# Kernel tuning notes

Measured on AMD Instinct MI355X. Metric: run time of the kernel, lower is better.

## Reference

```python
import jax, jax.numpy as jnp
import numpy as np

NUM_WINDOWS = 162   # icosphere order-2 windows
NUM_HEADS = 8

def layernorm(x, g, b, eps=1e-5):
    m = jnp.mean(x, axis=-1, keepdims=True)
    v = jnp.var(x, axis=-1, keepdims=True)
    return (x - m) * jax.lax.rsqrt(v + eps) * g + b

def setup_inputs() -> dict:
    key = jax.random.key(0)
    ks = jax.random.split(key, 16)
    B, N, C = 1, 41472, 512
    H, hid = NUM_HEADS, 4 * 512
    s = 0.02
    # window assignment: 162 windows x 256 vertices, shuffled (gather-based partition)
    rng = np.random.default_rng(0)
    wid = np.repeat(np.arange(NUM_WINDOWS), N // NUM_WINDOWS)
    rng.shuffle(wid)
    return {
        "x": jax.random.normal(ks[0], (B, N, C), jnp.float32),
        "mesh": jax.random.normal(ks[1], (N, 3), jnp.float32),
        "ln1_g": jnp.ones((C,), jnp.float32),
        "ln1_b": jnp.zeros((C,), jnp.float32),
        "qkv_w": jax.random.normal(ks[2], (C, 3 * C), jnp.float32) * s,
        "qkv_b": jnp.zeros((3 * C,), jnp.float32),
        "rel_bias": jax.random.normal(ks[3], (H, 1, 1), jnp.float32) * s,
        "proj_w": jax.random.normal(ks[4], (C, C), jnp.float32) * s,
        "proj_b": jnp.zeros((C,), jnp.float32),
        "ln2_g": jnp.ones((C,), jnp.float32),
        "ln2_b": jnp.zeros((C,), jnp.float32),
        "ffn_w1": jax.random.normal(ks[5], (C, hid), jnp.float32) * s,
        "ffn_b1": jnp.zeros((hid,), jnp.float32),
        "ffn_w2": jax.random.normal(ks[6], (hid, C), jnp.float32) * s,
        "ffn_b2": jnp.zeros((C,), jnp.float32),
        "window_ids": jnp.asarray(wid, dtype=jnp.int32),
    }

def reference(x, mesh, ln1_g, ln1_b, qkv_w, qkv_b, rel_bias, proj_w, proj_b,
              ln2_g, ln2_b, ffn_w1, ffn_b1, ffn_w2, ffn_b2, window_ids):
    B, N, C = x.shape
    H = NUM_HEADS
    hd = C // H
    ws = N // NUM_WINDOWS
    # --- gather-based window partition ---
    idx = jnp.argsort(window_ids)                      # [N]
    w = x[:, idx, :].reshape(B * NUM_WINDOWS, ws, C)   # [BW, ws, C]
    # --- window attention on norm1(windows) ---
    h = layernorm(w, ln1_g, ln1_b)
    qkv = (h @ qkv_w + qkv_b).reshape(B * NUM_WINDOWS, ws, 3, H, hd)
    q, k, v = qkv[:, :, 0], qkv[:, :, 1], qkv[:, :, 2]  # [BW, ws, H, hd]
    scale = hd ** -0.5
    attn = jnp.einsum('wqhd,wkhd->whqk', q, k) * scale + rel_bias
    attn = jax.nn.softmax(attn, axis=-1)
    out = jnp.einsum('whqk,wkhd->wqhd', attn, v).reshape(B * NUM_WINDOWS, ws, C)
    out = out @ proj_w + proj_b
    # --- reverse partition + residual ---
    inv = jnp.argsort(idx)
    x = x + out.reshape(B, N, C)[:, inv, :]
    # --- FFN block ---
    h2 = layernorm(x, ln2_g, ln2_b)
    f = jax.nn.gelu(h2 @ ffn_w1 + ffn_b1, approximate=False) @ ffn_w2 + ffn_b2
    x = x + f
    return (x, mesh)
```

## Files before the change

kernel.cpp:

```cpp
#include <hip/hip_runtime.h>
#include <hip/hip_bf16.h>
#include <math.h>

#define NW   162
#define WS   256
#define NH   8
#define HD   64
#define CC   512
#define NTOK 41472
#define HID  2048

typedef __bf16 bf16x8 __attribute__((ext_vector_type(8)));
typedef float  floatx4 __attribute__((ext_vector_type(4)));

__device__ __forceinline__ void gload_lds16(const __bf16* g, __bf16* l) {
    __builtin_amdgcn_global_load_lds((const __attribute__((address_space(1))) void*)g,
                                     (__attribute__((address_space(3))) void*)l,
                                     16, 0, 0);
}
__device__ __forceinline__ float fast_rcp(float x) { return __builtin_amdgcn_rcpf(x); }

__global__ __launch_bounds__(256)
void build_perm_atomic(const int* __restrict__ wid, int* __restrict__ perm,
                       int* __restrict__ pos, int* __restrict__ counters) {
    const int i = blockIdx.x * 256 + threadIdx.x;
    const int w = wid[i];
    const int r = atomicAdd(&counters[w], 1);
    perm[w * WS + r] = i;
    pos[i] = w * WS + r;
}

__global__ void transpose_bf16(const float* __restrict__ in,
                               __bf16* __restrict__ out, int K, int N) {
    int idx = blockIdx.x * 256 + threadIdx.x;
    if (idx >= K * N) return;
    int n = idx / K, k = idx - n * K;
    out[idx] = (__bf16)in[(size_t)k * N + n];
}

__global__ __launch_bounds__(64)
void ln1_gather(const float* __restrict__ x, const int* __restrict__ perm,
                const float* __restrict__ g, const float* __restrict__ b,
                __bf16* __restrict__ h) {
    const int j = blockIdx.x, lane = threadIdx.x;
    const int orig = perm[j];
    const float4* xp = (const float4*)(x + (size_t)orig * CC);
    float4 a0 = xp[lane * 2 + 0], a1 = xp[lane * 2 + 1];
    float s  = a0.x + a0.y + a0.z + a0.w + a1.x + a1.y + a1.z + a1.w;
    float sq = a0.x*a0.x + a0.y*a0.y + a0.z*a0.z + a0.w*a0.w
             + a1.x*a1.x + a1.y*a1.y + a1.z*a1.z + a1.w*a1.w;
#pragma unroll
    for (int o = 32; o; o >>= 1) { s += __shfl_xor(s, o); sq += __shfl_xor(sq, o); }
    const float m  = s * (1.f / CC);
    const float rs = rsqrtf(sq * (1.f / CC) - m * m + 1e-5f);
    const float4* g4 = (const float4*)g;  const float4* b4 = (const float4*)b;
    float4 g0 = g4[lane*2+0], g1 = g4[lane*2+1], bb0 = b4[lane*2+0], bb1 = b4[lane*2+1];
    bf16x8 o8;
    o8[0] = (__bf16)((a0.x - m) * rs * g0.x + bb0.x);
    o8[1] = (__bf16)((a0.y - m) * rs * g0.y + bb0.y);
    o8[2] = (__bf16)((a0.z - m) * rs * g0.z + bb0.z);
    o8[3] = (__bf16)((a0.w - m) * rs * g0.w + bb0.w);
    o8[4] = (__bf16)((a1.x - m) * rs * g1.x + bb1.x);
    o8[5] = (__bf16)((a1.y - m) * rs * g1.y + bb1.y);
    o8[6] = (__bf16)((a1.z - m) * rs * g1.z + bb1.z);
    o8[7] = (__bf16)((a1.w - m) * rs * g1.w + bb1.w);
    *(bf16x8*)(h + (size_t)j * CC + lane * 8) = o8;
}

__global__ __launch_bounds__(64)
void resid_ln2(const float* __restrict__ x, const float* __restrict__ ptmp,
               const int* __restrict__ pos, const float* __restrict__ g,
               const float* __restrict__ b, float* __restrict__ xout,
               __bf16* __restrict__ h2) {
    const int i = blockIdx.x, lane = threadIdx.x;
    const int p = pos[i];
    const float4* xp = (const float4*)(x + (size_t)i * CC);
    const float4* pp = (const float4*)(ptmp + (size_t)p * CC);
    float4 a0 = xp[lane*2+0], a1 = xp[lane*2+1];
    float4 t0 = pp[lane*2+0], t1 = pp[lane*2+1];
    a0.x += t0.x; a0.y += t0.y; a0.z += t0.z; a0.w += t0.w;
    a1.x += t1.x; a1.y += t1.y; a1.z += t1.z; a1.w += t1.w;
    float4* op = (float4*)(xout + (size_t)i * CC);
    op[lane*2+0] = a0; op[lane*2+1] = a1;
    float s  = a0.x + a0.y + a0.z + a0.w + a1.x + a1.y + a1.z + a1.w;
    float sq = a0.x*a0.x + a0.y*a0.y + a0.z*a0.z + a0.w*a0.w
             + a1.x*a1.x + a1.y*a1.y + a1.z*a1.z + a1.w*a1.w;
#pragma unroll
    for (int o = 32; o; o >>= 1) { s += __shfl_xor(s, o); sq += __shfl_xor(sq, o); }
    const float m  = s * (1.f / CC);
    const float rs = rsqrtf(sq * (1.f / CC) - m * m + 1e-5f);
    const float4* g4 = (const float4*)g;  const float4* b4 = (const float4*)b;
    float4 g0 = g4[lane*2+0], g1 = g4[lane*2+1], bb0 = b4[lane*2+0], bb1 = b4[lane*2+1];
    bf16x8 o8;
    o8[0] = (__bf16)((a0.x - m) * rs * g0.x + bb0.x);
    o8[1] = (__bf16)((a0.y - m) * rs * g0.y + bb0.y);
    o8[2] = (__bf16)((a0.z - m) * rs * g0.z + bb0.z);
    o8[3] = (__bf16)((a0.w - m) * rs * g0.w + bb0.w);
    o8[4] = (__bf16)((a1.x - m) * rs * g1.x + bb1.x);
    o8[5] = (__bf16)((a1.y - m) * rs * g1.y + bb1.y);
    o8[6] = (__bf16)((a1.z - m) * rs * g1.z + bb1.z);
    o8[7] = (__bf16)((a1.w - m) * rs * g1.w + bb1.w);
    *(bf16x8*)(h2 + (size_t)i * CC + lane * 8) = o8;
}

template <int EPI>
__global__ __launch_bounds__(256)
void gemm_bt(const __bf16* __restrict__ A, const __bf16* __restrict__ Bt,
             const float* __restrict__ bias, const float* __restrict__ res,
             float* __restrict__ Cf, __bf16* __restrict__ Cb,
             int M, int N, int K) {
    __shared__ __bf16 As[128 * 64];
    __shared__ __bf16 Bs[128 * 64];
    const int tid = threadIdx.x;
    const int wave = tid >> 6, lane = tid & 63;
    const int wm = wave & 1, wn = wave >> 1;
    const int bm = blockIdx.y, bn = blockIdx.x;
    const int lr = lane & 15, lq = lane >> 4;

    floatx4 acc[4][4];
#pragma unroll
    for (int i = 0; i < 4; i++)
#pragma unroll
        for (int j = 0; j < 4; j++) acc[i][j] = (floatx4){0.f, 0.f, 0.f, 0.f};

    const int srow = tid >> 3;
    const int sseg = (tid & 7) ^ (srow & 7);
    const __bf16* gA = A  + (size_t)(bm * 128 + srow) * K + sseg * 8;
    const __bf16* gB = Bt + (size_t)(bn * 128 + srow) * K + sseg * 8;
    __bf16* lA = As + (size_t)(wave * 64) * 8;
    __bf16* lB = Bs + (size_t)(wave * 64) * 8;

    for (int kt = 0; kt < K; kt += 64) {
        __syncthreads();
#pragma unroll
        for (int j = 0; j < 4; j++) {
            gload_lds16(gA + (size_t)(j * 32) * K + kt, lA + j * 2048);
            gload_lds16(gB + (size_t)(j * 32) * K + kt, lB + j * 2048);
        }
        __syncthreads();
#pragma unroll
        for (int kk = 0; kk < 2; kk++) {
            bf16x8 af[4], bfr[4];
#pragma unroll
            for (int mt = 0; mt < 4; mt++)
                af[mt] = *(const bf16x8*)(As + (wm * 64 + mt * 16 + lr) * 64 +
                                          (((kk * 4 + lq) ^ (lr & 7)) * 8));
#pragma unroll
            for (int nt = 0; nt < 4; nt++)
                bfr[nt] = *(const bf16x8*)(Bs + (wn * 64 + nt * 16 + lr) * 64 +
                                           (((kk * 4 + lq) ^ (lr & 7)) * 8));
#pragma unroll
            for (int mt = 0; mt < 4; mt++)
#pragma unroll
                for (int nt = 0; nt < 4; nt++)
                    acc[mt][nt] = __builtin_amdgcn_mfma_f32_16x16x32_bf16(
                        af[mt], bfr[nt], acc[mt][nt], 0, 0, 0);
        }
    }

    if constexpr (EPI == 0 || EPI == 2) {
        __syncthreads();
        __bf16* rb = wm ? Bs : As;
#pragma unroll
        for (int mt = 0; mt < 4; mt++)
#pragma unroll
            for (int nt = 0; nt < 4; nt++) {
                const int cl = wn * 64 + nt * 16 + lr;
                const float bv = bias[bn * 128 + cl];
#pragma unroll
                for (int r = 0; r < 4; r++) {
                    float v = acc[mt][nt][r] + bv;
                    if constexpr (EPI == 2) {
                        const float e = __expf(v * -1.702f);
                        v = v * fast_rcp(1.f + e);
                    }
                    rb[(mt * 16 + lq * 4 + r) * 128 + cl] = (__bf16)v;
                }
            }
        __syncthreads();
#pragma unroll
        for (int j = 0; j < 8; j++) {
            const int c = j * 256 + tid;
            const __bf16* reg = (j < 4) ? As : Bs;
            const int rc = c & 1023;
            const int row = rc >> 4, seg = rc & 15;
            bf16x8 val = *(const bf16x8*)(reg + row * 128 + seg * 8);
            *(bf16x8*)(Cb + (size_t)(bm * 128 + (j >> 2) * 64 + row) * N +
                       bn * 128 + seg * 8) = val;
        }
    } else {
#pragma unroll
        for (int mt = 0; mt < 4; mt++) {
            const int row = bm * 128 + wm * 64 + mt * 16 + lq * 4;
#pragma unroll
            for (int nt = 0; nt < 4; nt++) {
                const int col = bn * 128 + wn * 64 + nt * 16 + lr;
                const float bv = bias[col];
#pragma unroll
                for (int r = 0; r < 4; r++) {
                    float v = acc[mt][nt][r] + bv;
                    const size_t off = (size_t)(row + r) * N + col;
                    if constexpr (EPI == 1) Cf[off] = v;
                    else                    Cf[off] = res[off] + v;
                }
            }
        }
    }
}

__global__ __launch_bounds__(256)
void attn_mfma(const __bf16* __restrict__ qkv, __bf16* __restrict__ aout,
               const float* __restrict__ rel_bias) {
    __shared__ __bf16 vsT[HD * WS];
    __shared__ __bf16 pbuf[4][64][34];
    const int w = blockIdx.x, h = blockIdx.y;
    const int tid = threadIdx.x;
    const int wave = tid >> 6, lane = tid & 63;
    const int lr = lane & 15, lq = lane >> 4;
    const size_t base = (size_t)w * (WS * 1536) + h * 64;

    for (int c = tid; c < WS * 8; c += 256) {
        const int key = c >> 3, d8 = c & 7;
        bf16x8 vv = *(const bf16x8*)(qkv + base + 1024 + (size_t)key * 1536 + d8 * 8);
#pragma unroll
        for (int jj = 0; jj < 8; jj++) {
            const int d = d8 * 8 + jj;
            vsT[d * WS + (((key >> 3) ^ (d & 31)) << 3) + (key & 7)] = vv[jj];
        }
    }

    const int q0 = wave * 64;
    bf16x8 qf[4][2];
#pragma unroll
    for (int mt = 0; mt < 4; mt++)
#pragma unroll
        for (int kk = 0; kk < 2; kk++)
            qf[mt][kk] = *(const bf16x8*)(qkv + base +
                (size_t)(q0 + mt * 16 + lr) * 1536 + kk * 32 + lq * 8);

    __syncthreads();

    floatx4 o[4][4];
    float lsum[4][4];
#pragma unroll
    for (int mt = 0; mt < 4; mt++)
#pragma unroll
        for (int dt = 0; dt < 4; dt++) o[mt][dt] = (floatx4){0.f, 0.f, 0.f, 0.f};
#pragma unroll
    for (int mt = 0; mt < 4; mt++)
#pragma unroll
        for (int r = 0; r < 4; r++) lsum[mt][r] = 0.f;

    const float sc = 0.125f * 1.44269504089f;
    const float bb = rel_bias[h] * 1.44269504089f;
    const __bf16* kp0 = qkv + base + 512;

    bf16x8 kc[2][2];
#pragma unroll
    for (int nt = 0; nt < 2; nt++) {
        const __bf16* kp = kp0 + (size_t)(nt * 16 + lr) * 1536 + lq * 8;
        kc[nt][0] = *(const bf16x8*)(kp);
        kc[nt][1] = *(const bf16x8*)(kp + 32);
    }

    for (int kt = 0; kt < 8; kt++) {
        const int kbase = kt * 32;
        bf16x8 kn[2][2];
        if (kt < 7) {
#pragma unroll
            for (int nt = 0; nt < 2; nt++) {
                const __bf16* kp = kp0 + (size_t)(kbase + 32 + nt * 16 + lr) * 1536 + lq * 8;
                kn[nt][0] = *(const bf16x8*)(kp);
                kn[nt][1] = *(const bf16x8*)(kp + 32);
            }
        }
        floatx4 s[4][2];
#pragma unroll
        for (int mt = 0; mt < 4; mt++)
#pragma unroll
            for (int nt = 0; nt < 2; nt++) s[mt][nt] = (floatx4){0.f, 0.f, 0.f, 0.f};
#pragma unroll
        for (int nt = 0; nt < 2; nt++)
#pragma unroll
            for (int mt = 0; mt < 4; mt++) {
                s[mt][nt] = __builtin_amdgcn_mfma_f32_16x16x32_bf16(qf[mt][0], kc[nt][0], s[mt][nt], 0, 0, 0);
                s[mt][nt] = __builtin_amdgcn_mfma_f32_16x16x32_bf16(qf[mt][1], kc[nt][1], s[mt][nt], 0, 0, 0);
            }
#pragma unroll
        for (int mt = 0; mt < 4; mt++)
#pragma unroll
            for (int nt = 0; nt < 2; nt++)
#pragma unroll
                for (int r = 0; r < 4; r++) {
                    float e = exp2f(s[mt][nt][r] * sc + bb);
                    lsum[mt][r] += e;
                    pbuf[wave][mt * 16 + lq * 4 + r][nt * 16 + lr] = (__bf16)e;
                }
        bf16x8 vf[4];
#pragma unroll
        for (int dt = 0; dt < 4; dt++) {
            const int d = dt * 16 + lr;
            vf[dt] = *(const bf16x8*)(vsT + d * WS +
                                      (((kt * 4 + lq) ^ (d & 31)) << 3));
        }
#pragma unroll
        for (int mt = 0; mt < 4; mt++) {
            bf16x8 pf = *(const bf16x8*)(&pbuf[wave][mt * 16 + lr][lq * 8]);
#pragma unroll
            for (int dt = 0; dt < 4; dt++)
                o[mt][dt] = __builtin_amdgcn_mfma_f32_16x16x32_bf16(pf, vf[dt], o[mt][dt], 0, 0, 0);
        }
#pragma unroll
        for (int nt = 0; nt < 2; nt++) { kc[nt][0] = kn[nt][0]; kc[nt][1] = kn[nt][1]; }
    }

#pragma unroll
    for (int mt = 0; mt < 4; mt++)
#pragma unroll
        for (int r = 0; r < 4; r++) {
            float v = lsum[mt][r];
            v += __shfl_xor(v, 1); v += __shfl_xor(v, 2);
            v += __shfl_xor(v, 4); v += __shfl_xor(v, 8);
            lsum[mt][r] = fast_rcp(v);
        }

#pragma unroll
    for (int dh = 0; dh < 2; dh++) {
#pragma unroll
        for (int mt = 0; mt < 4; mt++)
#pragma unroll
            for (int dt = 0; dt < 2; dt++)
#pragma unroll
                for (int r = 0; r < 4; r++)
                    pbuf[wave][mt * 16 + lq * 4 + r][dt * 16 + lr] =
                        (__bf16)(o[mt][dh * 2 + dt][r] * lsum[mt][r]);
#pragma unroll
        for (int it = 0; it < 4; it++) {
            const int c = it * 64 + lane;
            const int row = c >> 2, seg = c & 3;
            bf16x8 val = *(const bf16x8*)(&pbuf[wave][row][seg * 8]);
            *(bf16x8*)(aout + (size_t)(w * WS + q0 + row) * CC + h * 64 + dh * 32 + seg * 8) = val;
        }
    }
}

extern "C" void kernel_launch(void* const* d_in, const int* in_sizes, int n_in,
                              void* d_out, int out_size, void* d_ws, size_t ws_size,
                              hipStream_t stream) {
    const float* x      = (const float*)d_in[0];
    const float* mesh   = (const float*)d_in[1];
    const float* ln1_g  = (const float*)d_in[2];
    const float* ln1_b  = (const float*)d_in[3];
    const float* qkv_w  = (const float*)d_in[4];
    const float* qkv_b  = (const float*)d_in[5];
    const float* rel_b  = (const float*)d_in[6];
    const float* proj_w = (const float*)d_in[7];
    const float* proj_b = (const float*)d_in[8];
    const float* ln2_g  = (const float*)d_in[9];
    const float* ln2_b  = (const float*)d_in[10];
    const float* w1     = (const float*)d_in[11];
    const float* b1     = (const float*)d_in[12];
    const float* w2     = (const float*)d_in[13];
    const float* b2     = (const float*)d_in[14];
    const int*   wid    = (const int*)d_in[15];

    char* ws = (char*)d_ws;
    int*    perm  = (int*)(ws + 0);
    int*    pos   = (int*)(ws + 165888);
    __bf16* wqkv  = (__bf16*)(ws + 331776);
    __bf16* wproj = (__bf16*)(ws + 1904640);
    __bf16* w1t   = (__bf16*)(ws + 2428928);
    __bf16* w2t   = (__bf16*)(ws + 4526080);
    const size_t BB = 6623232;
    __bf16* hln1 = (__bf16*)(ws + BB);
    __bf16* qkv  = (__bf16*)(ws + BB + 42467328);
    __bf16* aout = (__bf16*)(ws + BB + 169869312);
    float*  ptmp = (float*)(ws + BB);
    __bf16* h2   = (__bf16*)(ws + BB + 84934656);
    __bf16* f1   = (__bf16*)(ws + BB + 127401984);
    float*  xout = (float*)d_out;
    int*    counters = (int*)aout;

    hipMemsetAsync(counters, 0, NW * sizeof(int), stream);
    build_perm_atomic<<<NTOK / 256, 256, 0, stream>>>(wid, perm, pos, counters);

    transpose_bf16<<<(512 * 1536 + 255) / 256, 256, 0, stream>>>(qkv_w, wqkv, 512, 1536);
    transpose_bf16<<<(512 * 512 + 255) / 256, 256, 0, stream>>>(proj_w, wproj, 512, 512);
    transpose_bf16<<<(512 * 2048 + 255) / 256, 256, 0, stream>>>(w1, w1t, 512, 2048);
    transpose_bf16<<<(2048 * 512 + 255) / 256, 256, 0, stream>>>(w2, w2t, 2048, 512);

    ln1_gather<<<NTOK, 64, 0, stream>>>(x, perm, ln1_g, ln1_b, hln1);

    gemm_bt<0><<<dim3(1536 / 128, NTOK / 128), 256, 0, stream>>>(
        hln1, wqkv, qkv_b, nullptr, nullptr, qkv, NTOK, 1536, 512);

    attn_mfma<<<dim3(NW, NH), 256, 0, stream>>>(qkv, aout, rel_b);

    gemm_bt<1><<<dim3(512 / 128, NTOK / 128), 256, 0, stream>>>(
        aout, wproj, proj_b, nullptr, ptmp, nullptr, NTOK, 512, 512);

    resid_ln2<<<NTOK, 64, 0, stream>>>(x, ptmp, pos, ln2_g, ln2_b, xout, h2);

    gemm_bt<2><<<dim3(2048 / 128, NTOK / 128), 256, 0, stream>>>(
        h2, w1t, b1, nullptr, nullptr, f1, NTOK, 2048, 512);

    gemm_bt<3><<<dim3(512 / 128, NTOK / 128), 256, 0, stream>>>(
        f1, w2t, b2, xout, xout, nullptr, NTOK, 512, 2048);

    hipMemcpyAsync((char*)d_out + (size_t)NTOK * CC * 4, mesh,
                   (size_t)NTOK * 3 * 4, hipMemcpyDeviceToDevice, stream);
}
```

Baseline: 798.0 us.

## Replace GEMM with 256x256-tile double-buffered, phase-interleaved MFMA kernel

Replaces the 128x128, 4-wave GEMM with a 256x256-tile, 8-wave kernel that double-buffers A and B tiles in 128 KB of LDS. It splits each K-step into four MFMA quadrants, interleaving async global-to-LDS loads with compute using explicit vmcnt waits, barriers and setprio. It also remaps workgroup IDs so that neighbouring tiles land on the same XCD for L2 reuse. The aim is to hide load latency, raise arithmetic intensity and improve cache locality. The cost is more registers and LDS per block, which limits occupancy, and smaller grids for the N=512 GEMMs.

Result: faster. 768.5 us (-3.7%).

```diff
diff --git a/kernel.cpp b/kernel.cpp
--- a/kernel.cpp
+++ b/kernel.cpp
@@ -19,6 +19,11 @@
                                      16, 0, 0);
 }
 __device__ __forceinline__ float fast_rcp(float x) { return __builtin_amdgcn_rcpf(x); }
+
+#define GBAR()  __builtin_amdgcn_s_barrier()
+#define VMW(N)  asm volatile("s_waitcnt vmcnt(" #N ")" ::: "memory")
+#define LGKM0() asm volatile("s_waitcnt lgkmcnt(0)" ::: "memory")
+#define SCHED0() __builtin_amdgcn_sched_barrier(0)
 
 __global__ __launch_bounds__(256)
 void build_perm_atomic(const int* __restrict__ wid, int* __restrict__ perm,
@@ -103,102 +108,182 @@
     *(bf16x8*)(h2 + (size_t)i * CC + lane * 8) = o8;
 }
 
+__device__ __forceinline__ void stage_A(const __bf16* __restrict__ g, int K, int kcol,
+                                        __bf16* lds, int h, int tid, int wave) {
+    const int sch = ((tid & 7) ^ ((tid >> 3) & 7)) << 3;
+#pragma unroll
+    for (int j = 0; j < 2; j++) {
+        const int rw   = (j * 512 + tid) >> 3;
+        const int row  = (rw & 63) + ((rw & 64) << 1) + (h << 6);
+        const int rw0  = j * 64 + wave * 8;
+        const int row0 = (rw0 & 63) + ((rw0 & 64) << 1) + (h << 6);
+        gload_lds16(g + (size_t)row * K + kcol + sch, lds + row0 * 64);
+    }
+}
+__device__ __forceinline__ void stage_B(const __bf16* __restrict__ g, int K, int kcol,
+                                        __bf16* lds, int h, int tid, int wave) {
+    const int sch = ((tid & 7) ^ ((tid >> 3) & 7)) << 3;
+#pragma unroll
+    for (int j = 0; j < 2; j++) {
+        const int rw   = (j * 512 + tid) >> 3;
+        const int row  = (rw & 31) + ((rw >> 5) << 6) + (h << 5);
+        const int rw0  = j * 64 + wave * 8;
+        const int row0 = (rw0 & 31) + ((rw0 >> 5) << 6) + (h << 5);
+        gload_lds16(g + (size_t)row * K + kcol + sch, lds + row0 * 64);
+    }
+}
+
+__device__ __forceinline__ void load_afr(const __bf16* buf, int wm, int mh,
+                                         int lr, int lq, bf16x8 (&af)[4][2]) {
+#pragma unroll
+    for (int mt = 0; mt < 4; mt++) {
+        const __bf16* rp = buf + (wm * 128 + mh * 64 + mt * 16 + lr) * 64;
+#pragma unroll
+        for (int kk = 0; kk < 2; kk++)
+            af[mt][kk] = *(const bf16x8*)(rp + (((kk * 4 + lq) ^ (lr & 7)) << 3));
+    }
+}
+__device__ __forceinline__ void load_bfr(const __bf16* buf, int wn, int nh,
+                                         int lr, int lq, bf16x8 (&bf)[2][2]) {
+#pragma unroll
+    for (int nt = 0; nt < 2; nt++) {
+        const __bf16* rp = buf + (wn * 64 + nh * 32 + nt * 16 + lr) * 64;
+#pragma unroll
+        for (int kk = 0; kk < 2; kk++)
+            bf[nt][kk] = *(const bf16x8*)(rp + (((kk * 4 + lq) ^ (lr & 7)) << 3));
+    }
+}
+
+#define MFMA_QUAD(MH, NH, AF, BF)                                              \
+    _Pragma("unroll") for (int kk_ = 0; kk_ < 2; kk_++)                        \
+    _Pragma("unroll") for (int mt_ = 0; mt_ < 4; mt_++)                        \
+    _Pragma("unroll") for (int nt_ = 0; nt_ < 2; nt_++)                        \
+        acc[(MH) * 4 + mt_][(NH) * 2 + nt_] =                                  \
+            __builtin_amdgcn_mfma_f32_16x16x32_bf16(                           \
+                AF[mt_][kk_], BF[nt_][kk_],                                    \
+                acc[(MH) * 4 + mt_][(NH) * 2 + nt_], 0, 0, 0);
+
 template <int EPI>
-__global__ __launch_bounds__(256)
-void gemm_bt(const __bf16* __restrict__ A, const __bf16* __restrict__ Bt,
+__global__ __launch_bounds__(512, 2)
+void gemm256(const __bf16* __restrict__ A, const __bf16* __restrict__ Bt,
              const float* __restrict__ bias, const float* __restrict__ res,
              float* __restrict__ Cf, __bf16* __restrict__ Cb,
              int M, int N, int K) {
-    __shared__ __bf16 As[128 * 64];
-    __shared__ __bf16 Bs[128 * 64];
-    const int tid = threadIdx.x;
-    const int wave = tid >> 6, lane = tid & 63;
-    const int wm = wave & 1, wn = wave >> 1;
-    const int bm = blockIdx.y, bn = blockIdx.x;
+    __shared__ __bf16 smem[65536];
+    __bf16* Ac = smem;
+    __bf16* An = smem + 16384;
+    __bf16* Bc = smem + 32768;
+    __bf16* Bn = smem + 49152;
+
+    const int tid  = threadIdx.x;
+    const int wave = tid >> 6;
+    const int lane = tid & 63;
+    const int wm = wave >> 2, wn = wave & 3;
     const int lr = lane & 15, lq = lane >> 4;
 
-    floatx4 acc[4][4];
-#pragma unroll
-    for (int i = 0; i < 4; i++)
+    const int gx  = gridDim.x;
+    const int nwg = gx * gridDim.y;
+    const int orig = blockIdx.y * gx + blockIdx.x;
+    const int q8 = nwg >> 3, r8 = nwg & 7;
+    const int xcd = orig & 7, oi = orig >> 3;
+    const int wgid = (xcd < r8 ? xcd * (q8 + 1) : r8 * (q8 + 1) + (xcd - r8) * q8) + oi;
+    const int bm = wgid / gx, bn = wgid - bm * gx;
+
+    const __bf16* gA = A  + (size_t)bm * 256 * K;
+    const __bf16* gB = Bt + (size_t)bn * 256 * K;
+    const int NT = K >> 6;
+
+    floatx4 acc[8][4];
+#pragma unroll
+    for (int i = 0; i < 8; i++)
 #pragma unroll
         for (int j = 0; j < 4; j++) acc[i][j] = (floatx4){0.f, 0.f, 0.f, 0.f};
 
-    const int srow = tid >> 3;
-    const int sseg = (tid & 7) ^ (srow & 7);
-    const __bf16* gA = A  + (size_t)(bm * 128 + srow) * K + sseg * 8;
-    const __bf16* gB = Bt + (size_t)(bn * 128 + srow) * K + sseg * 8;
-    __bf16* lA = As + (size_t)(wave * 64) * 8;
-    __bf16* lB = Bs + (size_t)(wave * 64) * 8;
-
-    for (int kt = 0; kt < K; kt += 64) {
-        __syncthreads();
-#pragma unroll
-        for (int j = 0; j < 4; j++) {
-            gload_lds16(gA + (size_t)(j * 32) * K + kt, lA + j * 2048);
-            gload_lds16(gB + (size_t)(j * 32) * K + kt, lB + j * 2048);
-        }
-        __syncthreads();
-#pragma unroll
-        for (int kk = 0; kk < 2; kk++) {
-            bf16x8 af[4], bfr[4];
-#pragma unroll
-            for (int mt = 0; mt < 4; mt++)
-                af[mt] = *(const bf16x8*)(As + (wm * 64 + mt * 16 + lr) * 64 +
-                                          (((kk * 4 + lq) ^ (lr & 7)) * 8));
-#pragma unroll
-            for (int nt = 0; nt < 4; nt++)
-                bfr[nt] = *(const bf16x8*)(Bs + (wn * 64 + nt * 16 + lr) * 64 +
-                                           (((kk * 4 + lq) ^ (lr & 7)) * 8));
-#pragma unroll
-            for (int mt = 0; mt < 4; mt++)
-#pragma unroll
-                for (int nt = 0; nt < 4; nt++)
-                    acc[mt][nt] = __builtin_amdgcn_mfma_f32_16x16x32_bf16(
-                        af[mt], bfr[nt], acc[mt][nt], 0, 0, 0);
-        }
+    stage_A(gA, K, 0, Ac, 0, tid, wave);
+    stage_B(gB, K, 0, Bc, 0, tid, wave);
+    stage_B(gB, K, 0, Bc, 1, tid, wave);
+    stage_A(gA, K, 0, Ac, 1, tid, wave);
+    if (NT > 1) stage_A(gA, K, 64, An, 0, tid, wave);
+    VMW(4);
+    GBAR();
+
+    bf16x8 af[4][2], b0[2][2], b1[2][2];
+
+    for (int t = 0; t < NT; t++) {
+        const int k1 = (t + 1) << 6;
+        if (t == NT - 1) { VMW(0); } else { VMW(4); }
+        if (t + 1 < NT) stage_B(gB, K, k1, Bn, 0, tid, wave);
+        load_afr(Ac, wm, 0, lr, lq, af);
+        load_bfr(Bc, wn, 0, lr, lq, b0);
+        GBAR(); LGKM0(); SCHED0();
+        __builtin_amdgcn_s_setprio(1);
+        MFMA_QUAD(0, 0, af, b0);
+        __builtin_amdgcn_s_setprio(0);
+        GBAR();
+        VMW(4);
+        if (t + 1 < NT) stage_B(gB, K, k1, Bn, 1, tid, wave);
+        load_bfr(Bc, wn, 1, lr, lq, b1);
+        GBAR(); LGKM0(); SCHED0();
+        __builtin_amdgcn_s_setprio(1);
+        MFMA_QUAD(0, 1, af, b1);
+        __builtin_amdgcn_s_setprio(0);
+        GBAR();
+        VMW(4);
+        if (t + 1 < NT) stage_A(gA, K, k1, An, 1, tid, wave);
+        load_afr(Ac, wm, 1, lr, lq, af);
+        GBAR(); LGKM0(); SCHED0();
+        __builtin_amdgcn_s_setprio(1);
+        MFMA_QUAD(1, 1, af, b1);
+        __builtin_amdgcn_s_setprio(0);
+        GBAR();
+        VMW(4);
+        if (t + 2 < NT) stage_A(gA, K, (t + 2) << 6, Ac, 0, tid, wave);
+        GBAR();
+        __builtin_amdgcn_s_setprio(1);
+        MFMA_QUAD(1, 0, af, b0);
+        __builtin_amdgcn_s_setprio(0);
+        GBAR();
+        __bf16* ta = Ac; Ac = An; An = ta;
+        __bf16* tb = Bc; Bc = Bn; Bn = tb;
     }
 
     if constexpr (EPI == 0 || EPI == 2) {
-        __syncthreads();
-        __bf16* rb = wm ? Bs : As;
-#pragma unroll
-        for (int mt = 0; mt < 4; mt++)
-#pragma unroll
-            for (int nt = 0; nt < 4; nt++) {
-                const int cl = wn * 64 + nt * 16 + lr;
-                const float bv = bias[bn * 128 + cl];
+        __bf16* Ct = smem;
+#pragma unroll
+        for (int m = 0; m < 8; m++)
+#pragma unroll
+            for (int n = 0; n < 4; n++) {
+                const int col = wn * 64 + n * 16 + lr;
+                const float bv = bias[bn * 256 + col];
 #pragma unroll
                 for (int r = 0; r < 4; r++) {
-                    float v = acc[mt][nt][r] + bv;
+                    float v = acc[m][n][r] + bv;
                     if constexpr (EPI == 2) {
                         const float e = __expf(v * -1.702f);
                         v = v * fast_rcp(1.f + e);
                     }
-                    rb[(mt * 16 + lq * 4 + r) * 128 + cl] = (__bf16)v;
+                    Ct[(wm * 128 + m * 16 + lq * 4 + r) * 256 + col] = (__bf16)v;
                 }
             }
         __syncthreads();
 #pragma unroll
-        for (int j = 0; j < 8; j++) {
-            const int c = j * 256 + tid;
-            const __bf16* reg = (j < 4) ? As : Bs;
-            const int rc = c & 1023;
-            const int row = rc >> 4, seg = rc & 15;
-            bf16x8 val = *(const bf16x8*)(reg + row * 128 + seg * 8);
-            *(bf16x8*)(Cb + (size_t)(bm * 128 + (j >> 2) * 64 + row) * N +
-                       bn * 128 + seg * 8) = val;
+        for (int j = 0; j < 16; j++) {
+            const int ci = j * 512 + tid;
+            const int row = ci >> 5, ch = ci & 31;
+            *(bf16x8*)(Cb + (size_t)(bm * 256 + row) * N + bn * 256 + ch * 8) =
+                *(const bf16x8*)(Ct + row * 256 + ch * 8);
         }
     } else {
 #pragma unroll
-        for (int mt = 0; mt < 4; mt++) {
-            const int row = bm * 128 + wm * 64 + mt * 16 + lq * 4;
-#pragma unroll
-            for (int nt = 0; nt < 4; nt++) {
-                const int col = bn * 128 + wn * 64 + nt * 16 + lr;
+        for (int m = 0; m < 8; m++) {
+            const int row = bm * 256 + wm * 128 + m * 16 + lq * 4;
+#pragma unroll
+            for (int n = 0; n < 4; n++) {
+                const int col = bn * 256 + wn * 64 + n * 16 + lr;
                 const float bv = bias[col];
 #pragma unroll
                 for (int r = 0; r < 4; r++) {
-                    float v = acc[mt][nt][r] + bv;
+                    const float v = acc[m][n][r] + bv;
                     const size_t off = (size_t)(row + r) * N + col;
                     if constexpr (EPI == 1) Cf[off] = v;
                     else                    Cf[off] = res[off] + v;
@@ -391,20 +476,20 @@
 
     ln1_gather<<<NTOK, 64, 0, stream>>>(x, perm, ln1_g, ln1_b, hln1);
 
-    gemm_bt<0><<<dim3(1536 / 128, NTOK / 128), 256, 0, stream>>>(
+    gemm256<0><<<dim3(1536 / 256, NTOK / 256), 512, 0, stream>>>(
         hln1, wqkv, qkv_b, nullptr, nullptr, qkv, NTOK, 1536, 512);
 
     attn_mfma<<<dim3(NW, NH), 256, 0, stream>>>(qkv, aout, rel_b);
 
-    gemm_bt<1><<<dim3(512 / 128, NTOK / 128), 256, 0, stream>>>(
+    gemm256<1><<<dim3(512 / 256, NTOK / 256), 512, 0, stream>>>(
         aout, wproj, proj_b, nullptr, ptmp, nullptr, NTOK, 512, 512);
 
     resid_ln2<<<NTOK, 64, 0, stream>>>(x, ptmp, pos, ln2_g, ln2_b, xout, h2);
 
-    gemm_bt<2><<<dim3(2048 / 128, NTOK / 128), 256, 0, stream>>>(
+    gemm256<2><<<dim3(2048 / 256, NTOK / 256), 512, 0, stream>>>(
         h2, w1t, b1, nullptr, nullptr, f1, NTOK, 2048, 512);
 
-    gemm_bt<3><<<dim3(512 / 128, NTOK / 128), 256, 0, stream>>>(
+    gemm256<3><<<dim3(512 / 256, NTOK / 256), 512, 0, stream>>>(
         f1, w2t, b2, xout, xout, nullptr, NTOK, 512, 2048);
 
     hipMemcpyAsync((char*)d_out + (size_t)NTOK * CC * 4, mesh,
```
